# Performance work log

Hardware: AMD Instinct MI355X
Metric: run time of the kernel (lower is better)

The kernel has to match this reference:

```python
import jax, jax.numpy as jnp
import numpy as np

N, E, D, L = 50000, 400000, 128, 5
EPS = 1e-5  # BatchNorm1d default eps


def setup_inputs() -> dict:
    key = jax.random.key(0)
    ks = jax.random.split(key, 9)
    x = jax.random.normal(ks[0], (N, D), jnp.float32)
    edge_index = jax.random.randint(ks[1], (2, E), 0, N)
    edge_attr = jax.random.normal(ks[2], (E, 4), jnp.float32)
    # per-layer params (stacked over L layers)
    W1 = jax.random.normal(ks[3], (L, 3, D), jnp.float32) * (6.0 / (3 + D)) ** 0.5
    W2 = jax.random.normal(ks[4], (L, 1, D), jnp.float32) * (6.0 / (1 + D)) ** 0.5
    Wm = jax.random.normal(ks[5], (L, D, 2 * D), jnp.float32) * (6.0 / (3 * D)) ** 0.5
    bm = jnp.zeros((L, D), jnp.float32)
    gamma = jnp.ones((L, D), jnp.float32)
    beta = jnp.zeros((L, D), jnp.float32)
    return dict(x=x, edge_index=edge_index, edge_attr=edge_attr,
                W1=W1, W2=W2, Wm=Wm, bm=bm, gamma=gamma, beta=beta)


def reference(x, edge_index, edge_attr, W1, W2, Wm, bm, gamma, beta):
    row, col = edge_index[0], edge_index[1]
    # symmetric GCN norm: deg computed by scattering ones at col
    deg = jax.ops.segment_sum(jnp.ones((E,), x.dtype), col, num_segments=N)
    deg_safe = jnp.where(deg > 0, deg, 1.0)
    dinv = jnp.where(deg > 0, deg_safe ** -0.5, 0.0)  # [N]
    norm = dinv[row] * dinv[col]                      # [E]

    h = x
    for l in range(L):
        # edge feature projection ('2-3d'): first 3 cols @ W1 + last col @ W2
        edge_fea = edge_attr[:, :3] @ W1[l] + edge_attr[:, 3:] @ W2[l]  # [E, D]
        # message: norm * (x_j + edge_fea), gather at source (row)
        msg = norm[:, None] * (h[row] + edge_fea)                       # [E, D]
        # aggregate: scatter-add at target (col)
        agg = jax.ops.segment_sum(msg, col, num_segments=N)             # [N, D]
        # mlp(concat([x, out])) with ReLU
        h2 = jax.nn.relu(jnp.concatenate([h, agg], axis=1) @ Wm[l].T + bm[l])
        # BatchNorm1d (training mode: batch stats, biased variance)
        mean = h2.mean(axis=0)
        var = jnp.mean((h2 - mean) ** 2, axis=0)
        h = gamma[l] * (h2 - mean) * jax.lax.rsqrt(var + EPS) + beta[l]
        if l < L - 1:
            h = jax.nn.relu(h)
        # dropout p=0 -> identity
    return h
```

## Files before the change

### kernel.cpp

```cpp
#include <hip/hip_runtime.h>

#define D 128
#define EPSBN 1e-5f
#define PB 800

typedef __attribute__((ext_vector_type(8))) short bf16x8;
typedef __attribute__((ext_vector_type(4))) float f32x4;

static __device__ __forceinline__ unsigned short f2b(float f) {
    unsigned u = __float_as_uint(f);
    unsigned r = u + 0x7FFF + ((u >> 16) & 1);
    return (unsigned short)(r >> 16);
}
static __device__ __forceinline__ float b2f_lo(unsigned p) { return __uint_as_float(p << 16); }
static __device__ __forceinline__ float b2f_hi(unsigned p) { return __uint_as_float(p & 0xFFFF0000u); }


__global__ void k_deg(const int* __restrict__ ei, int E, int* __restrict__ deg) {
    int e = blockIdx.x * 256 + threadIdx.x;
    if (e < E) atomicAdd(&deg[ei[E + e]], 1);
}

__global__ void k_dinv(const int* __restrict__ deg, float* __restrict__ dinv, int N) {
    int v = blockIdx.x * 256 + threadIdx.x;
    if (v < N) {
        int d = deg[v];
        dinv[v] = (d > 0) ? rsqrtf((float)d) : 0.0f;
    }
}

__global__ void k_bsum(const int* __restrict__ deg, int* __restrict__ bsum, int N) {
    __shared__ int sm[256];
    int t = threadIdx.x, v = blockIdx.x * 256 + t;
    sm[t] = (v < N) ? deg[v] : 0;
    __syncthreads();
    for (int off = 128; off > 0; off >>= 1) {
        if (t < off) sm[t] += sm[t + off];
        __syncthreads();
    }
    if (t == 0) bsum[blockIdx.x] = sm[0];
}

__global__ void k_bscan(const int* __restrict__ bsum, int* __restrict__ boff,
                        int* __restrict__ row_ptr, int NB, int N, int E) {
    __shared__ int sm[256];
    int t = threadIdx.x;
    int v = (t < NB) ? bsum[t] : 0;
    sm[t] = v;
    __syncthreads();
    for (int off = 1; off < 256; off <<= 1) {
        int x = (t >= off) ? sm[t - off] : 0;
        __syncthreads();
        sm[t] += x;
        __syncthreads();
    }
    if (t < NB) boff[t] = sm[t] - v;
    if (t == 0) row_ptr[N] = E;
}

__global__ void k_scatter(const int* __restrict__ deg, const int* __restrict__ boff,
                          int* __restrict__ row_ptr, int* __restrict__ cursor, int N) {
    __shared__ int sm[256];
    int t = threadIdx.x, v = blockIdx.x * 256 + t;
    int val = (v < N) ? deg[v] : 0;
    sm[t] = val;
    __syncthreads();
    for (int off = 1; off < 256; off <<= 1) {
        int x = (t >= off) ? sm[t - off] : 0;
        __syncthreads();
        sm[t] += x;
        __syncthreads();
    }
    if (v < N) {
        int e = boff[blockIdx.x] + sm[t] - val;
        row_ptr[v] = e;
        cursor[v] = e;
    }
}

__global__ void k_fill(const int* __restrict__ ei, int* __restrict__ cursor,
                       int2* __restrict__ csr, int E) {
    int e = blockIdx.x * 256 + threadIdx.x;
    if (e >= E) return;
    int r = ei[e], c = ei[E + e];
    int pos = atomicAdd(&cursor[c], 1);
    csr[pos] = make_int2(r, e);
}

__global__ void k_cvals(const int* __restrict__ row_ptr, int2* __restrict__ csr,
                        const float* __restrict__ dinv, const float* __restrict__ attr,
                        float4* __restrict__ cvals, int N) {
    int v = blockIdx.x * 256 + threadIdx.x;
    if (v >= N) return;
    float dv = dinv[v];
    int jb = row_ptr[v], je = row_ptr[v + 1];
    float4 acc = make_float4(0.f, 0.f, 0.f, 0.f);
    for (int j = jb; j < je; ++j) {
        int2 e = csr[j];
        float nm = dinv[e.x] * dv;
        float4 a = *(const float4*)(attr + (size_t)e.y * 4);
        acc.x += nm * a.x; acc.y += nm * a.y;
        acc.z += nm * a.z; acc.w += nm * a.w;
        csr[j] = make_int2(e.x, __float_as_int(nm));
    }
    cvals[v] = acc;
}

__global__ void k_cvt(const float* __restrict__ in, unsigned short* __restrict__ outp, int n4) {
    int i = blockIdx.x * 256 + threadIdx.x;
    if (i >= n4) return;
    float4 v = *(const float4*)(in + (size_t)i * 4);
    ushort4 p;
    p.x = f2b(v.x); p.y = f2b(v.y); p.z = f2b(v.z); p.w = f2b(v.w);
    *(ushort4*)(outp + (size_t)i * 4) = p;
}


__global__ __launch_bounds__(256) void k_spmm(
        const unsigned short* __restrict__ hb, const int* __restrict__ row_ptr,
        const int2* __restrict__ csr, const float4* __restrict__ cvals,
        const float* __restrict__ W1l, const float* __restrict__ W2l,
        unsigned short* __restrict__ aggb, int N) {
    int lane = threadIdx.x & 63;
    int v = blockIdx.x * 4 + (threadIdx.x >> 6);
    if (v >= N) return;
    int qw = lane >> 4;
    int l4 = lane & 15;
    int d0 = l4 * 8;
    int jb = row_ptr[v], je = row_ptr[v + 1];

    float a[8];
#pragma unroll
    for (int i = 0; i < 8; ++i) a[i] = 0.f;

    for (int j0 = jb; j0 < je; j0 += 4) {
        int j = j0 + qw;
        bool ok = (j < je);
        int2 e = csr[ok ? j : jb];
        float nm = ok ? __int_as_float(e.y) : 0.f;
        uint4 p = *(const uint4*)(hb + (size_t)e.x * D + d0);
        a[0] += nm * b2f_lo(p.x); a[1] += nm * b2f_hi(p.x);
        a[2] += nm * b2f_lo(p.y); a[3] += nm * b2f_hi(p.y);
        a[4] += nm * b2f_lo(p.z); a[5] += nm * b2f_hi(p.z);
        a[6] += nm * b2f_lo(p.w); a[7] += nm * b2f_hi(p.w);
    }
#pragma unroll
    for (int i = 0; i < 8; ++i) {
        a[i] += __shfl_xor(a[i], 16);
        a[i] += __shfl_xor(a[i], 32);
    }
    if (qw == 0) {
        float4 c = cvals[v];
        float4 wa0 = *(const float4*)(W1l + d0);
        float4 wa1 = *(const float4*)(W1l + d0 + 4);
        float4 wb0 = *(const float4*)(W1l + D + d0);
        float4 wb1 = *(const float4*)(W1l + D + d0 + 4);
        float4 wc0 = *(const float4*)(W1l + 2 * D + d0);
        float4 wc1 = *(const float4*)(W1l + 2 * D + d0 + 4);
        float4 wd0 = *(const float4*)(W2l + d0);
        float4 wd1 = *(const float4*)(W2l + d0 + 4);
        a[0] += c.x * wa0.x + c.y * wb0.x + c.z * wc0.x + c.w * wd0.x;
        a[1] += c.x * wa0.y + c.y * wb0.y + c.z * wc0.y + c.w * wd0.y;
        a[2] += c.x * wa0.z + c.y * wb0.z + c.z * wc0.z + c.w * wd0.z;
        a[3] += c.x * wa0.w + c.y * wb0.w + c.z * wc0.w + c.w * wd0.w;
        a[4] += c.x * wa1.x + c.y * wb1.x + c.z * wc1.x + c.w * wd1.x;
        a[5] += c.x * wa1.y + c.y * wb1.y + c.z * wc1.y + c.w * wd1.y;
        a[6] += c.x * wa1.z + c.y * wb1.z + c.z * wc1.z + c.w * wd1.z;
        a[7] += c.x * wa1.w + c.y * wb1.w + c.z * wc1.w + c.w * wd1.w;
        uint4 o;
        o.x = ((unsigned)f2b(a[1]) << 16) | (unsigned)f2b(a[0]);
        o.y = ((unsigned)f2b(a[3]) << 16) | (unsigned)f2b(a[2]);
        o.z = ((unsigned)f2b(a[5]) << 16) | (unsigned)f2b(a[4]);
        o.w = ((unsigned)f2b(a[7]) << 16) | (unsigned)f2b(a[6]);
        *(uint4*)(aggb + (size_t)v * D + d0) = o;
    }
}

#define GROWS 64
#define GBK 64
__global__ __launch_bounds__(256) void k_gemm(
        const unsigned short* __restrict__ hb, const unsigned short* __restrict__ aggb,
        const unsigned short* __restrict__ Wmb, const float* __restrict__ bml,
        float* __restrict__ h2, float* __restrict__ pbuf, int N) {
    __shared__ unsigned short As[GROWS][GBK + 8];
    __shared__ unsigned short Bs[D][GBK + 8];
    __shared__ float sred[2][4][D];
    int tid = threadIdx.x;
    int lane = tid & 63, wave = tid >> 6;
    int n0 = blockIdx.x * GROWS;
    int l15 = lane & 15, q = lane >> 4;
    f32x4 acc[8];
#pragma unroll
    for (int t = 0; t < 8; ++t) acc[t] = (f32x4){0.f, 0.f, 0.f, 0.f};

    for (int kc = 0; kc < 4; ++kc) {
        const unsigned short* src = (kc < 2) ? hb : aggb;
        int k0 = (kc & 1) * GBK;
#pragma unroll
        for (int i = 0; i < 2; ++i) {
            int idx = tid + i * 256;
            int r = idx >> 3, seg = idx & 7;
            uint4 val = make_uint4(0u, 0u, 0u, 0u);
            if (n0 + r < N) val = *(const uint4*)(src + (size_t)(n0 + r) * D + k0 + seg * 8);
            *(uint4*)&As[r][seg * 8] = val;
        }
#pragma unroll
        for (int i = 0; i < 4; ++i) {
            int idx = tid + i * 256;
            int n = idx >> 3, seg = idx & 7;
            *(uint4*)&Bs[n][seg * 8] =
                *(const uint4*)(Wmb + (size_t)n * 256 + kc * GBK + seg * 8);
        }
        __syncthreads();
#pragma unroll
        for (int s = 0; s < 2; ++s) {
            bf16x8 a = *(const bf16x8*)&As[wave * 16 + l15][s * 32 + q * 8];
#pragma unroll
            for (int t = 0; t < 8; ++t) {
                bf16x8 b = *(const bf16x8*)&Bs[t * 16 + l15][s * 32 + q * 8];
                acc[t] = __builtin_amdgcn_mfma_f32_16x16x32_bf16(a, b, acc[t], 0, 0, 0);
            }
        }
        __syncthreads();
    }
    bool full = (n0 + GROWS <= N);
    float ps[8], pq[8];
#pragma unroll
    for (int t = 0; t < 8; ++t) {
        int n = t * 16 + l15;
        float bias = bml[n];
        float s = 0.f, qs = 0.f;
#pragma unroll
        for (int r = 0; r < 4; ++r) {
            int m = n0 + wave * 16 + q * 4 + r;
            float v = fmaxf(acc[t][r] + bias, 0.f);
            if (full || m < N) {
                h2[(size_t)m * D + n] = v;
                s += v; qs += v * v;
            }
        }
        ps[t] = s; pq[t] = qs;
    }
#pragma unroll
    for (int t = 0; t < 8; ++t) {
        ps[t] += __shfl_xor(ps[t], 16); ps[t] += __shfl_xor(ps[t], 32);
        pq[t] += __shfl_xor(pq[t], 16); pq[t] += __shfl_xor(pq[t], 32);
    }
    if (q == 0) {
#pragma unroll
        for (int t = 0; t < 8; ++t) {
            sred[0][wave][t * 16 + l15] = ps[t];
            sred[1][wave][t * 16 + l15] = pq[t];
        }
    }
    __syncthreads();
    if (tid < D) {
        float s = sred[0][0][tid] + sred[0][1][tid] + sred[0][2][tid] + sred[0][3][tid];
        pbuf[(size_t)tid * PB + blockIdx.x] = s;
    } else {
        int n = tid - D;
        float qv = sred[1][0][n] + sred[1][1][n] + sred[1][2][n] + sred[1][3][n];
        pbuf[(size_t)(n + D) * PB + blockIdx.x] = qv;
    }
}

__global__ __launch_bounds__(128) void k_reduce(
        const float* __restrict__ pbuf, const float* __restrict__ gam,
        const float* __restrict__ bet, float* __restrict__ scsh, int nb, int N) {
    int n = blockIdx.x;
    int t = threadIdx.x;
    float s = 0.f, qv = 0.f;
    for (int b = t; b < nb; b += 128) {
        s  += pbuf[(size_t)n * PB + b];
        qv += pbuf[(size_t)(n + D) * PB + b];
    }
#pragma unroll
    for (int off = 32; off > 0; off >>= 1) {
        s += __shfl_down(s, off);
        qv += __shfl_down(qv, off);
    }
    __shared__ float aux[4];
    if ((t & 63) == 0) { aux[t >> 6] = s; aux[2 + (t >> 6)] = qv; }
    __syncthreads();
    if (t == 0) {
        float S = aux[0] + aux[1], Q = aux[2] + aux[3];
        float mean = S / (float)N;
        float var = fmaxf(Q / (float)N - mean * mean, 0.f);
        float sc = gam[n] * rsqrtf(var + EPSBN);
        scsh[n] = sc;
        scsh[D + n] = bet[n] - mean * sc;
    }
}

__global__ void k_norm(const float* __restrict__ h2, const float* __restrict__ scsh,
                       unsigned short* __restrict__ hb_out, float* __restrict__ out_f,
                       int total4, int last) {
    int i = blockIdx.x * 256 + threadIdx.x;
    if (i >= total4) return;
    int base = i * 4;
    int d = base & (D - 1);
    float4 v = *(const float4*)(h2 + base);
    float4 o;
    o.x = scsh[d + 0] * v.x + scsh[D + d + 0];
    o.y = scsh[d + 1] * v.y + scsh[D + d + 1];
    o.z = scsh[d + 2] * v.z + scsh[D + d + 2];
    o.w = scsh[d + 3] * v.w + scsh[D + d + 3];
    if (!last) {
        o.x = fmaxf(o.x, 0.f); o.y = fmaxf(o.y, 0.f);
        o.z = fmaxf(o.z, 0.f); o.w = fmaxf(o.w, 0.f);
        ushort4 p;
        p.x = f2b(o.x); p.y = f2b(o.y); p.z = f2b(o.z); p.w = f2b(o.w);
        *(ushort4*)(hb_out + base) = p;
    } else {
        *(float4*)(out_f + base) = o;
    }
}


extern "C" void kernel_launch(void* const* d_in, const int* in_sizes, int n_in,
                              void* d_out, int out_size, void* d_ws, size_t ws_size,
                              hipStream_t stream) {
    const float* x    = (const float*)d_in[0];
    const int*   ei   = (const int*)d_in[1];
    const float* attr = (const float*)d_in[2];
    const float* W1   = (const float*)d_in[3];
    const float* W2   = (const float*)d_in[4];
    const float* Wm   = (const float*)d_in[5];
    const float* bm   = (const float*)d_in[6];
    const float* gam  = (const float*)d_in[7];
    const float* bet  = (const float*)d_in[8];
    float* out = (float*)d_out;

    const int N = in_sizes[0] / D;
    const int E = in_sizes[1] / 2;
    const int L = in_sizes[3] / (3 * D);
    const int NB = (N + 255) / 256;

    size_t off = 0;
    auto carve = [&](size_t bytes) {
        void* p = (char*)d_ws + off;
        off += (bytes + 255) & ~(size_t)255;
        return p;
    };
    int*            deg     = (int*)carve((size_t)N * 4);
    float*          dinv    = (float*)carve((size_t)N * 4);
    int*            row_ptr = (int*)carve((size_t)(N + 1) * 4);
    int*            cursor  = (int*)carve((size_t)N * 4);
    int*            bsum    = (int*)carve((size_t)NB * 4);
    int*            boff    = (int*)carve((size_t)NB * 4);
    int2*           csr     = (int2*)carve((size_t)(E + 4) * 8);
    float4*         cvals   = (float4*)carve((size_t)N * 16);
    unsigned short* xb      = (unsigned short*)carve((size_t)N * D * 2);
    unsigned short* hb      = (unsigned short*)carve((size_t)N * D * 2);
    unsigned short* aggb    = (unsigned short*)carve((size_t)N * D * 2);
    unsigned short* Wmb     = (unsigned short*)carve((size_t)L * D * 256 * 2);
    float*          h2      = (float*)carve((size_t)N * D * 4);
    float*          pbuf    = (float*)carve((size_t)2 * D * PB * 4);
    float*          scsh    = (float*)carve((size_t)2 * D * 4);
    (void)ws_size;

    hipMemsetAsync(deg, 0, (size_t)N * 4, stream);

    const int eb = (E + 255) / 256;
    k_deg<<<eb, 256, 0, stream>>>(ei, E, deg);
    k_dinv<<<NB, 256, 0, stream>>>(deg, dinv, N);
    k_bsum<<<NB, 256, 0, stream>>>(deg, bsum, N);
    k_bscan<<<1, 256, 0, stream>>>(bsum, boff, row_ptr, NB, N, E);
    k_scatter<<<NB, 256, 0, stream>>>(deg, boff, row_ptr, cursor, N);
    k_fill<<<eb, 256, 0, stream>>>(ei, cursor, csr, E);
    k_cvals<<<NB, 256, 0, stream>>>(row_ptr, csr, dinv, attr, cvals, N);

    const int xq = N * D / 4;
    k_cvt<<<(xq + 255) / 256, 256, 0, stream>>>(x, xb, xq);
    const int wq = L * D * 256 / 4;
    k_cvt<<<(wq + 255) / 256, 256, 0, stream>>>(Wm, Wmb, wq);

    const int total4 = N * D / 4;
    const int normb = (total4 + 255) / 256;
    const int gemmb = (N + GROWS - 1) / GROWS;
    const int spmmb = (N + 3) / 4;

    for (int l = 0; l < L; ++l) {
        const unsigned short* in = (l == 0) ? xb : hb;
        const float* W1l = W1 + (size_t)l * 3 * D;
        const float* W2l = W2 + (size_t)l * D;
        const unsigned short* Wml = Wmb + (size_t)l * D * 256;
        const float* bml = bm + (size_t)l * D;

        k_spmm<<<spmmb, 256, 0, stream>>>(in, row_ptr, csr, cvals, W1l, W2l, aggb, N);
        k_gemm<<<gemmb, 256, 0, stream>>>(in, aggb, Wml, bml, h2, pbuf, N);
        k_reduce<<<D, 128, 0, stream>>>(pbuf, gam + (size_t)l * D,
                                        bet + (size_t)l * D, scsh, gemmb, N);
        k_norm<<<normb, 256, 0, stream>>>(h2, scsh, hb, out, total4, (l < L - 1) ? 0 : 1);
    }
}
```

Before: 467.5 us.

## Fuse BatchNorm affine+ReLU into next layer's SpMM and GEMM loads

Drops the per-layer normalize kernel. The GEMM now stores the pre-norm activation as bf16, and the next layer's SpMM gather and GEMM A-tile load apply the BN scale/shift and ReLU on the fly. Only the last layer writes fp32 and runs a final normalize pass. This removes a full fp32 read and a bf16 write of the activation per layer, and halves the h2 write size. In exchange, the affine is recomputed once per edge in the gather, and bf16 rounding now happens before the normalization. Separately, CSR construction records the atomic slot in k_deg so a non-atomic placement kernel replaces the cursor atomics, and the SpMM loop is unrolled to two edges per quarter-wave.

```diff
diff --git a/kernel.cpp b/kernel.cpp
--- a/kernel.cpp
+++ b/kernel.cpp
@@ -16,9 +16,10 @@
 static __device__ __forceinline__ float b2f_hi(unsigned p) { return __uint_as_float(p & 0xFFFF0000u); }
 
 
-__global__ void k_deg(const int* __restrict__ ei, int E, int* __restrict__ deg) {
+__global__ void k_deg(const int* __restrict__ ei, int E, int* __restrict__ deg,
+                      int* __restrict__ pos) {
     int e = blockIdx.x * 256 + threadIdx.x;
-    if (e < E) atomicAdd(&deg[ei[E + e]], 1);
+    if (e < E) pos[e] = atomicAdd(&deg[ei[E + e]], 1);
 }
 
 __global__ void k_dinv(const int* __restrict__ deg, float* __restrict__ dinv, int N) {
@@ -59,7 +60,7 @@
 }
 
 __global__ void k_scatter(const int* __restrict__ deg, const int* __restrict__ boff,
-                          int* __restrict__ row_ptr, int* __restrict__ cursor, int N) {
+                          int* __restrict__ row_ptr, int N) {
     __shared__ int sm[256];
     int t = threadIdx.x, v = blockIdx.x * 256 + t;
     int val = (v < N) ? deg[v] : 0;
@@ -71,20 +72,15 @@
         sm[t] += x;
         __syncthreads();
     }
-    if (v < N) {
-        int e = boff[blockIdx.x] + sm[t] - val;
-        row_ptr[v] = e;
-        cursor[v] = e;
-    }
-}
-
-__global__ void k_fill(const int* __restrict__ ei, int* __restrict__ cursor,
-                       int2* __restrict__ csr, int E) {
+    if (v < N) row_ptr[v] = boff[blockIdx.x] + sm[t] - val;
+}
+
+__global__ void k_place(const int* __restrict__ ei, const int* __restrict__ row_ptr,
+                        const int* __restrict__ pos, int2* __restrict__ csr, int E) {
     int e = blockIdx.x * 256 + threadIdx.x;
     if (e >= E) return;
-    int r = ei[e], c = ei[E + e];
-    int pos = atomicAdd(&cursor[c], 1);
-    csr[pos] = make_int2(r, e);
+    int c = ei[E + e];
+    csr[row_ptr[c] + pos[e]] = make_int2(ei[e], e);
 }
 
 __global__ void k_cvals(const int* __restrict__ row_ptr, int2* __restrict__ csr,
@@ -120,6 +116,7 @@
         const unsigned short* __restrict__ hb, const int* __restrict__ row_ptr,
         const int2* __restrict__ csr, const float4* __restrict__ cvals,
         const float* __restrict__ W1l, const float* __restrict__ W2l,
+        const float* __restrict__ scsh, int apply,
         unsigned short* __restrict__ aggb, int N) {
     int lane = threadIdx.x & 63;
     int v = blockIdx.x * 4 + (threadIdx.x >> 6);
@@ -133,16 +130,53 @@
 #pragma unroll
     for (int i = 0; i < 8; ++i) a[i] = 0.f;
 
-    for (int j0 = jb; j0 < je; j0 += 4) {
-        int j = j0 + qw;
-        bool ok = (j < je);
-        int2 e = csr[ok ? j : jb];
-        float nm = ok ? __int_as_float(e.y) : 0.f;
-        uint4 p = *(const uint4*)(hb + (size_t)e.x * D + d0);
-        a[0] += nm * b2f_lo(p.x); a[1] += nm * b2f_hi(p.x);
-        a[2] += nm * b2f_lo(p.y); a[3] += nm * b2f_hi(p.y);
-        a[4] += nm * b2f_lo(p.z); a[5] += nm * b2f_hi(p.z);
-        a[6] += nm * b2f_lo(p.w); a[7] += nm * b2f_hi(p.w);
+    if (apply) {
+        float sc[8], sh[8];
+#pragma unroll
+        for (int i = 0; i < 8; i += 4) {
+            float4 s = *(const float4*)(scsh + d0 + i);
+            float4 t = *(const float4*)(scsh + D + d0 + i);
+            sc[i] = s.x; sc[i + 1] = s.y; sc[i + 2] = s.z; sc[i + 3] = s.w;
+            sh[i] = t.x; sh[i + 1] = t.y; sh[i + 2] = t.z; sh[i + 3] = t.w;
+        }
+        for (int j0 = jb; j0 < je; j0 += 8) {
+            int ja = j0 + qw, jc = j0 + 4 + qw;
+            bool oa = (ja < je), oc = (jc < je);
+            int2 ea = csr[oa ? ja : jb];
+            int2 ec = csr[oc ? jc : jb];
+            float na = oa ? __int_as_float(ea.y) : 0.f;
+            float nc = oc ? __int_as_float(ec.y) : 0.f;
+            uint4 pa = *(const uint4*)(hb + (size_t)ea.x * D + d0);
+            uint4 pc = *(const uint4*)(hb + (size_t)ec.x * D + d0);
+            float xa[8] = {b2f_lo(pa.x), b2f_hi(pa.x), b2f_lo(pa.y), b2f_hi(pa.y),
+                           b2f_lo(pa.z), b2f_hi(pa.z), b2f_lo(pa.w), b2f_hi(pa.w)};
+            float xc[8] = {b2f_lo(pc.x), b2f_hi(pc.x), b2f_lo(pc.y), b2f_hi(pc.y),
+                           b2f_lo(pc.z), b2f_hi(pc.z), b2f_lo(pc.w), b2f_hi(pc.w)};
+#pragma unroll
+            for (int i = 0; i < 8; ++i) {
+                a[i] += na * fmaxf(sc[i] * xa[i] + sh[i], 0.f);
+                a[i] += nc * fmaxf(sc[i] * xc[i] + sh[i], 0.f);
+            }
+        }
+    } else {
+        for (int j0 = jb; j0 < je; j0 += 8) {
+            int ja = j0 + qw, jc = j0 + 4 + qw;
+            bool oa = (ja < je), oc = (jc < je);
+            int2 ea = csr[oa ? ja : jb];
+            int2 ec = csr[oc ? jc : jb];
+            float na = oa ? __int_as_float(ea.y) : 0.f;
+            float nc = oc ? __int_as_float(ec.y) : 0.f;
+            uint4 pa = *(const uint4*)(hb + (size_t)ea.x * D + d0);
+            uint4 pc = *(const uint4*)(hb + (size_t)ec.x * D + d0);
+            a[0] += na * b2f_lo(pa.x) + nc * b2f_lo(pc.x);
+            a[1] += na * b2f_hi(pa.x) + nc * b2f_hi(pc.x);
+            a[2] += na * b2f_lo(pa.y) + nc * b2f_lo(pc.y);
+            a[3] += na * b2f_hi(pa.y) + nc * b2f_hi(pc.y);
+            a[4] += na * b2f_lo(pa.z) + nc * b2f_lo(pc.z);
+            a[5] += na * b2f_hi(pa.z) + nc * b2f_hi(pc.z);
+            a[6] += na * b2f_lo(pa.w) + nc * b2f_lo(pc.w);
+            a[7] += na * b2f_hi(pa.w) + nc * b2f_hi(pc.w);
+        }
     }
 #pragma unroll
     for (int i = 0; i < 8; ++i) {
@@ -179,9 +213,11 @@
 #define GROWS 64
 #define GBK 64
 __global__ __launch_bounds__(256) void k_gemm(
-        const unsigned short* __restrict__ hb, const unsigned short* __restrict__ aggb,
+        const unsigned short* __restrict__ hsrc, const unsigned short* __restrict__ aggb,
         const unsigned short* __restrict__ Wmb, const float* __restrict__ bml,
-        float* __restrict__ h2, float* __restrict__ pbuf, int N) {
+        const float* __restrict__ scsh, int applyA,
+        unsigned short* __restrict__ h2b, float* __restrict__ h2f, int lastf,
+        float* __restrict__ pbuf, int N) {
     __shared__ unsigned short As[GROWS][GBK + 8];
     __shared__ unsigned short Bs[D][GBK + 8];
     __shared__ float sred[2][4][D];
@@ -194,7 +230,8 @@
     for (int t = 0; t < 8; ++t) acc[t] = (f32x4){0.f, 0.f, 0.f, 0.f};
 
     for (int kc = 0; kc < 4; ++kc) {
-        const unsigned short* src = (kc < 2) ? hb : aggb;
+        const unsigned short* src = (kc < 2) ? hsrc : aggb;
+        bool aff = (kc < 2) && applyA;
         int k0 = (kc & 1) * GBK;
 #pragma unroll
         for (int i = 0; i < 2; ++i) {
@@ -202,6 +239,25 @@
             int r = idx >> 3, seg = idx & 7;
             uint4 val = make_uint4(0u, 0u, 0u, 0u);
             if (n0 + r < N) val = *(const uint4*)(src + (size_t)(n0 + r) * D + k0 + seg * 8);
+            if (aff) {
+                int db = k0 + seg * 8;
+                float4 s0 = *(const float4*)(scsh + db);
+                float4 s1 = *(const float4*)(scsh + db + 4);
+                float4 t0 = *(const float4*)(scsh + D + db);
+                float4 t1 = *(const float4*)(scsh + D + db + 4);
+                float e0 = fmaxf(s0.x * b2f_lo(val.x) + t0.x, 0.f);
+                float e1 = fmaxf(s0.y * b2f_hi(val.x) + t0.y, 0.f);
+                float e2 = fmaxf(s0.z * b2f_lo(val.y) + t0.z, 0.f);
+                float e3 = fmaxf(s0.w * b2f_hi(val.y) + t0.w, 0.f);
+                float e4 = fmaxf(s1.x * b2f_lo(val.z) + t1.x, 0.f);
+                float e5 = fmaxf(s1.y * b2f_hi(val.z) + t1.y, 0.f);
+                float e6 = fmaxf(s1.z * b2f_lo(val.w) + t1.z, 0.f);
+                float e7 = fmaxf(s1.w * b2f_hi(val.w) + t1.w, 0.f);
+                val.x = ((unsigned)f2b(e1) << 16) | (unsigned)f2b(e0);
+                val.y = ((unsigned)f2b(e3) << 16) | (unsigned)f2b(e2);
+                val.z = ((unsigned)f2b(e5) << 16) | (unsigned)f2b(e4);
+                val.w = ((unsigned)f2b(e7) << 16) | (unsigned)f2b(e6);
+            }
             *(uint4*)&As[r][seg * 8] = val;
         }
 #pragma unroll
@@ -235,7 +291,8 @@
             int m = n0 + wave * 16 + q * 4 + r;
             float v = fmaxf(acc[t][r] + bias, 0.f);
             if (full || m < N) {
-                h2[(size_t)m * D + n] = v;
+                if (lastf) h2f[(size_t)m * D + n] = v;
+                else       h2b[(size_t)m * D + n] = f2b(v);
                 s += v; qs += v * v;
             }
         }
@@ -292,28 +349,19 @@
     }
 }
 
-__global__ void k_norm(const float* __restrict__ h2, const float* __restrict__ scsh,
-                       unsigned short* __restrict__ hb_out, float* __restrict__ out_f,
-                       int total4, int last) {
+__global__ void k_norm_last(const float* __restrict__ h2f, const float* __restrict__ scsh,
+                            float* __restrict__ out_f, int total4) {
     int i = blockIdx.x * 256 + threadIdx.x;
     if (i >= total4) return;
     int base = i * 4;
     int d = base & (D - 1);
-    float4 v = *(const float4*)(h2 + base);
+    float4 v = *(const float4*)(h2f + base);
     float4 o;
     o.x = scsh[d + 0] * v.x + scsh[D + d + 0];
     o.y = scsh[d + 1] * v.y + scsh[D + d + 1];
     o.z = scsh[d + 2] * v.z + scsh[D + d + 2];
     o.w = scsh[d + 3] * v.w + scsh[D + d + 3];
-    if (!last) {
-        o.x = fmaxf(o.x, 0.f); o.y = fmaxf(o.y, 0.f);
-        o.z = fmaxf(o.z, 0.f); o.w = fmaxf(o.w, 0.f);
-        ushort4 p;
-        p.x = f2b(o.x); p.y = f2b(o.y); p.z = f2b(o.z); p.w = f2b(o.w);
-        *(ushort4*)(hb_out + base) = p;
-    } else {
-        *(float4*)(out_f + base) = o;
-    }
+    *(float4*)(out_f + base) = o;
 }
 
 
@@ -345,16 +393,16 @@
     int*            deg     = (int*)carve((size_t)N * 4);
     float*          dinv    = (float*)carve((size_t)N * 4);
     int*            row_ptr = (int*)carve((size_t)(N + 1) * 4);
-    int*            cursor  = (int*)carve((size_t)N * 4);
+    int*            pos     = (int*)carve((size_t)E * 4);
     int*            bsum    = (int*)carve((size_t)NB * 4);
     int*            boff    = (int*)carve((size_t)NB * 4);
-    int2*           csr     = (int2*)carve((size_t)(E + 4) * 8);
+    int2*           csr     = (int2*)carve((size_t)(E + 8) * 8);
     float4*         cvals   = (float4*)carve((size_t)N * 16);
     unsigned short* xb      = (unsigned short*)carve((size_t)N * D * 2);
-    unsigned short* hb      = (unsigned short*)carve((size_t)N * D * 2);
+    unsigned short* h2b     = (unsigned short*)carve((size_t)N * D * 2);
     unsigned short* aggb    = (unsigned short*)carve((size_t)N * D * 2);
     unsigned short* Wmb     = (unsigned short*)carve((size_t)L * D * 256 * 2);
-    float*          h2      = (float*)carve((size_t)N * D * 4);
+    float*          h2f     = (float*)carve((size_t)N * D * 4);
     float*          pbuf    = (float*)carve((size_t)2 * D * PB * 4);
     float*          scsh    = (float*)carve((size_t)2 * D * 4);
     (void)ws_size;
@@ -362,12 +410,12 @@
     hipMemsetAsync(deg, 0, (size_t)N * 4, stream);
 
     const int eb = (E + 255) / 256;
-    k_deg<<<eb, 256, 0, stream>>>(ei, E, deg);
+    k_deg<<<eb, 256, 0, stream>>>(ei, E, deg, pos);
     k_dinv<<<NB, 256, 0, stream>>>(deg, dinv, N);
     k_bsum<<<NB, 256, 0, stream>>>(deg, bsum, N);
     k_bscan<<<1, 256, 0, stream>>>(bsum, boff, row_ptr, NB, N, E);
-    k_scatter<<<NB, 256, 0, stream>>>(deg, boff, row_ptr, cursor, N);
-    k_fill<<<eb, 256, 0, stream>>>(ei, cursor, csr, E);
+    k_scatter<<<NB, 256, 0, stream>>>(deg, boff, row_ptr, N);
+    k_place<<<eb, 256, 0, stream>>>(ei, row_ptr, pos, csr, E);
     k_cvals<<<NB, 256, 0, stream>>>(row_ptr, csr, dinv, attr, cvals, N);
 
     const int xq = N * D / 4;
@@ -376,21 +424,24 @@
     k_cvt<<<(wq + 255) / 256, 256, 0, stream>>>(Wm, Wmb, wq);
 
     const int total4 = N * D / 4;
-    const int normb = (total4 + 255) / 256;
     const int gemmb = (N + GROWS - 1) / GROWS;
     const int spmmb = (N + 3) / 4;
 
     for (int l = 0; l < L; ++l) {
-        const unsigned short* in = (l == 0) ? xb : hb;
+        const unsigned short* in = (l == 0) ? xb : h2b;
+        const int apply = (l > 0) ? 1 : 0;
+        const int last = (l == L - 1) ? 1 : 0;
         const float* W1l = W1 + (size_t)l * 3 * D;
         const float* W2l = W2 + (size_t)l * D;
         const unsigned short* Wml = Wmb + (size_t)l * D * 256;
         const float* bml = bm + (size_t)l * D;
 
-        k_spmm<<<spmmb, 256, 0, stream>>>(in, row_ptr, csr, cvals, W1l, W2l, aggb, N);
-        k_gemm<<<gemmb, 256, 0, stream>>>(in, aggb, Wml, bml, h2, pbuf, N);
+        k_spmm<<<spmmb, 256, 0, stream>>>(in, row_ptr, csr, cvals, W1l, W2l,
+                                          scsh, apply, aggb, N);
+        k_gemm<<<gemmb, 256, 0, stream>>>(in, aggb, Wml, bml, scsh, apply,
+                                          h2b, h2f, last, pbuf, N);
         k_reduce<<<D, 128, 0, stream>>>(pbuf, gam + (size_t)l * D,
                                         bet + (size_t)l * D, scsh, gemmb, N);
-        k_norm<<<normb, 256, 0, stream>>>(h2, scsh, hb, out, total4, (l < L - 1) ? 0 : 1);
-    }
-}
+    }
+    k_norm_last<<<(total4 + 255) / 256, 256, 0, stream>>>(h2f, scsh, out, total4);
+}
```

Measured after the change: 427.8 us. -8.5%, faster.

## Fuse SpMM aggregation into GEMM tile and simplify CSR build

Applied to the files above, without the earlier changes.

The per-layer SpMM is merged into the GEMM kernel. Each 64-row block gathers its neighbor aggregates into shared memory, so the aggb round trip through global memory and one launch per layer go away. The gather loop is unrolled to two edges per step to keep more loads in flight. CSR construction now records each edge's atomic slot during the degree pass and computes dinv inline, which drops the dinv and fill/cursor kernels. The risk is that the fused kernel has only about 782 blocks, each gathering serially over 16 rows per wave with larger shared memory, which may reduce parallelism and latency hiding compared with the 12500-block SpMM.

```diff
diff --git a/kernel.cpp b/kernel.cpp
--- a/kernel.cpp
+++ b/kernel.cpp
@@ -3,6 +3,8 @@
 #define D 128
 #define EPSBN 1e-5f
 #define PB 800
+#define GROWS 64
+#define GBK 64
 
 typedef __attribute__((ext_vector_type(8))) short bf16x8;
 typedef __attribute__((ext_vector_type(4))) float f32x4;
@@ -16,17 +18,10 @@
 static __device__ __forceinline__ float b2f_hi(unsigned p) { return __uint_as_float(p & 0xFFFF0000u); }
 
 
-__global__ void k_deg(const int* __restrict__ ei, int E, int* __restrict__ deg) {
+__global__ void k_deg(const int* __restrict__ ei, int E, int* __restrict__ deg,
+                      int* __restrict__ pos) {
     int e = blockIdx.x * 256 + threadIdx.x;
-    if (e < E) atomicAdd(&deg[ei[E + e]], 1);
-}
-
-__global__ void k_dinv(const int* __restrict__ deg, float* __restrict__ dinv, int N) {
-    int v = blockIdx.x * 256 + threadIdx.x;
-    if (v < N) {
-        int d = deg[v];
-        dinv[v] = (d > 0) ? rsqrtf((float)d) : 0.0f;
-    }
+    if (e < E) pos[e] = atomicAdd(&deg[ei[E + e]], 1);
 }
 
 __global__ void k_bsum(const int* __restrict__ deg, int* __restrict__ bsum, int N) {
@@ -59,7 +54,7 @@
 }
 
 __global__ void k_scatter(const int* __restrict__ deg, const int* __restrict__ boff,
-                          int* __restrict__ row_ptr, int* __restrict__ cursor, int N) {
+                          int* __restrict__ row_ptr, int N) {
     __shared__ int sm[256];
     int t = threadIdx.x, v = blockIdx.x * 256 + t;
     int val = (v < N) ? deg[v] : 0;
@@ -71,33 +66,31 @@
         sm[t] += x;
         __syncthreads();
     }
-    if (v < N) {
-        int e = boff[blockIdx.x] + sm[t] - val;
-        row_ptr[v] = e;
-        cursor[v] = e;
-    }
-}
-
-__global__ void k_fill(const int* __restrict__ ei, int* __restrict__ cursor,
-                       int2* __restrict__ csr, int E) {
+    if (v < N) row_ptr[v] = boff[blockIdx.x] + sm[t] - val;
+}
+
+__global__ void k_place(const int* __restrict__ ei, const int* __restrict__ row_ptr,
+                        const int* __restrict__ pos, int2* __restrict__ csr, int E) {
     int e = blockIdx.x * 256 + threadIdx.x;
     if (e >= E) return;
-    int r = ei[e], c = ei[E + e];
-    int pos = atomicAdd(&cursor[c], 1);
-    csr[pos] = make_int2(r, e);
+    int c = ei[E + e];
+    csr[row_ptr[c] + pos[e]] = make_int2(ei[e], e);
 }
 
 __global__ void k_cvals(const int* __restrict__ row_ptr, int2* __restrict__ csr,
-                        const float* __restrict__ dinv, const float* __restrict__ attr,
+                        const int* __restrict__ deg, const float* __restrict__ attr,
                         float4* __restrict__ cvals, int N) {
     int v = blockIdx.x * 256 + threadIdx.x;
     if (v >= N) return;
-    float dv = dinv[v];
+    int dgv = deg[v];
+    float dv = (dgv > 0) ? rsqrtf((float)dgv) : 0.f;
     int jb = row_ptr[v], je = row_ptr[v + 1];
     float4 acc = make_float4(0.f, 0.f, 0.f, 0.f);
     for (int j = jb; j < je; ++j) {
         int2 e = csr[j];
-        float nm = dinv[e.x] * dv;
+        int dgs = deg[e.x];
+        float ds = (dgs > 0) ? rsqrtf((float)dgs) : 0.f;
+        float nm = ds * dv;
         float4 a = *(const float4*)(attr + (size_t)e.y * 4);
         acc.x += nm * a.x; acc.y += nm * a.y;
         acc.z += nm * a.z; acc.w += nm * a.w;
@@ -116,72 +109,13 @@
 }
 
 
-__global__ __launch_bounds__(256) void k_spmm(
+__global__ __launch_bounds__(256) void k_fused(
         const unsigned short* __restrict__ hb, const int* __restrict__ row_ptr,
         const int2* __restrict__ csr, const float4* __restrict__ cvals,
         const float* __restrict__ W1l, const float* __restrict__ W2l,
-        unsigned short* __restrict__ aggb, int N) {
-    int lane = threadIdx.x & 63;
-    int v = blockIdx.x * 4 + (threadIdx.x >> 6);
-    if (v >= N) return;
-    int qw = lane >> 4;
-    int l4 = lane & 15;
-    int d0 = l4 * 8;
-    int jb = row_ptr[v], je = row_ptr[v + 1];
-
-    float a[8];
-#pragma unroll
-    for (int i = 0; i < 8; ++i) a[i] = 0.f;
-
-    for (int j0 = jb; j0 < je; j0 += 4) {
-        int j = j0 + qw;
-        bool ok = (j < je);
-        int2 e = csr[ok ? j : jb];
-        float nm = ok ? __int_as_float(e.y) : 0.f;
-        uint4 p = *(const uint4*)(hb + (size_t)e.x * D + d0);
-        a[0] += nm * b2f_lo(p.x); a[1] += nm * b2f_hi(p.x);
-        a[2] += nm * b2f_lo(p.y); a[3] += nm * b2f_hi(p.y);
-        a[4] += nm * b2f_lo(p.z); a[5] += nm * b2f_hi(p.z);
-        a[6] += nm * b2f_lo(p.w); a[7] += nm * b2f_hi(p.w);
-    }
-#pragma unroll
-    for (int i = 0; i < 8; ++i) {
-        a[i] += __shfl_xor(a[i], 16);
-        a[i] += __shfl_xor(a[i], 32);
-    }
-    if (qw == 0) {
-        float4 c = cvals[v];
-        float4 wa0 = *(const float4*)(W1l + d0);
-        float4 wa1 = *(const float4*)(W1l + d0 + 4);
-        float4 wb0 = *(const float4*)(W1l + D + d0);
-        float4 wb1 = *(const float4*)(W1l + D + d0 + 4);
-        float4 wc0 = *(const float4*)(W1l + 2 * D + d0);
-        float4 wc1 = *(const float4*)(W1l + 2 * D + d0 + 4);
-        float4 wd0 = *(const float4*)(W2l + d0);
-        float4 wd1 = *(const float4*)(W2l + d0 + 4);
-        a[0] += c.x * wa0.x + c.y * wb0.x + c.z * wc0.x + c.w * wd0.x;
-        a[1] += c.x * wa0.y + c.y * wb0.y + c.z * wc0.y + c.w * wd0.y;
-        a[2] += c.x * wa0.z + c.y * wb0.z + c.z * wc0.z + c.w * wd0.z;
-        a[3] += c.x * wa0.w + c.y * wb0.w + c.z * wc0.w + c.w * wd0.w;
-        a[4] += c.x * wa1.x + c.y * wb1.x + c.z * wc1.x + c.w * wd1.x;
-        a[5] += c.x * wa1.y + c.y * wb1.y + c.z * wc1.y + c.w * wd1.y;
-        a[6] += c.x * wa1.z + c.y * wb1.z + c.z * wc1.z + c.w * wd1.z;
-        a[7] += c.x * wa1.w + c.y * wb1.w + c.z * wc1.w + c.w * wd1.w;
-        uint4 o;
-        o.x = ((unsigned)f2b(a[1]) << 16) | (unsigned)f2b(a[0]);
-        o.y = ((unsigned)f2b(a[3]) << 16) | (unsigned)f2b(a[2]);
-        o.z = ((unsigned)f2b(a[5]) << 16) | (unsigned)f2b(a[4]);
-        o.w = ((unsigned)f2b(a[7]) << 16) | (unsigned)f2b(a[6]);
-        *(uint4*)(aggb + (size_t)v * D + d0) = o;
-    }
-}
-
-#define GROWS 64
-#define GBK 64
-__global__ __launch_bounds__(256) void k_gemm(
-        const unsigned short* __restrict__ hb, const unsigned short* __restrict__ aggb,
         const unsigned short* __restrict__ Wmb, const float* __restrict__ bml,
         float* __restrict__ h2, float* __restrict__ pbuf, int N) {
+    __shared__ unsigned short Ag[GROWS][D + 8];
     __shared__ unsigned short As[GROWS][GBK + 8];
     __shared__ unsigned short Bs[D][GBK + 8];
     __shared__ float sred[2][4][D];
@@ -189,20 +123,86 @@
     int lane = tid & 63, wave = tid >> 6;
     int n0 = blockIdx.x * GROWS;
     int l15 = lane & 15, q = lane >> 4;
+    int qw = q;
+    int l4 = l15;
+    int d0 = l4 * 8;
+
+    for (int i = 0; i < 16; ++i) {
+        int r = wave * 16 + i;
+        int v = n0 + r;
+        float a[8];
+#pragma unroll
+        for (int k = 0; k < 8; ++k) a[k] = 0.f;
+        if (v < N) {
+            int jb = row_ptr[v], je = row_ptr[v + 1];
+            for (int j0 = jb; j0 < je; j0 += 8) {
+                int ja = j0 + qw, jc = j0 + 4 + qw;
+                bool oa = (ja < je), oc = (jc < je);
+                int2 ea = csr[oa ? ja : jb];
+                int2 ec = csr[oc ? jc : jb];
+                float na = oa ? __int_as_float(ea.y) : 0.f;
+                float nc = oc ? __int_as_float(ec.y) : 0.f;
+                uint4 pa = *(const uint4*)(hb + (size_t)ea.x * D + d0);
+                uint4 pc = *(const uint4*)(hb + (size_t)ec.x * D + d0);
+                a[0] += na * b2f_lo(pa.x) + nc * b2f_lo(pc.x);
+                a[1] += na * b2f_hi(pa.x) + nc * b2f_hi(pc.x);
+                a[2] += na * b2f_lo(pa.y) + nc * b2f_lo(pc.y);
+                a[3] += na * b2f_hi(pa.y) + nc * b2f_hi(pc.y);
+                a[4] += na * b2f_lo(pa.z) + nc * b2f_lo(pc.z);
+                a[5] += na * b2f_hi(pa.z) + nc * b2f_hi(pc.z);
+                a[6] += na * b2f_lo(pa.w) + nc * b2f_lo(pc.w);
+                a[7] += na * b2f_hi(pa.w) + nc * b2f_hi(pc.w);
+            }
+#pragma unroll
+            for (int k = 0; k < 8; ++k) {
+                a[k] += __shfl_xor(a[k], 16);
+                a[k] += __shfl_xor(a[k], 32);
+            }
+            if (qw == 0) {
+                float4 c = cvals[v];
+                float4 wa0 = *(const float4*)(W1l + d0);
+                float4 wa1 = *(const float4*)(W1l + d0 + 4);
+                float4 wb0 = *(const float4*)(W1l + D + d0);
+                float4 wb1 = *(const float4*)(W1l + D + d0 + 4);
+                float4 wc0 = *(const float4*)(W1l + 2 * D + d0);
+                float4 wc1 = *(const float4*)(W1l + 2 * D + d0 + 4);
+                float4 wd0 = *(const float4*)(W2l + d0);
+                float4 wd1 = *(const float4*)(W2l + d0 + 4);
+                a[0] += c.x * wa0.x + c.y * wb0.x + c.z * wc0.x + c.w * wd0.x;
+                a[1] += c.x * wa0.y + c.y * wb0.y + c.z * wc0.y + c.w * wd0.y;
+                a[2] += c.x * wa0.z + c.y * wb0.z + c.z * wc0.z + c.w * wd0.z;
+                a[3] += c.x * wa0.w + c.y * wb0.w + c.z * wc0.w + c.w * wd0.w;
+                a[4] += c.x * wa1.x + c.y * wb1.x + c.z * wc1.x + c.w * wd1.x;
+                a[5] += c.x * wa1.y + c.y * wb1.y + c.z * wc1.y + c.w * wd1.y;
+                a[6] += c.x * wa1.z + c.y * wb1.z + c.z * wc1.z + c.w * wd1.z;
+                a[7] += c.x * wa1.w + c.y * wb1.w + c.z * wc1.w + c.w * wd1.w;
+            }
+        }
+        if (qw == 0) {
+            uint4 o;
+            o.x = ((unsigned)f2b(a[1]) << 16) | (unsigned)f2b(a[0]);
+            o.y = ((unsigned)f2b(a[3]) << 16) | (unsigned)f2b(a[2]);
+            o.z = ((unsigned)f2b(a[5]) << 16) | (unsigned)f2b(a[4]);
+            o.w = ((unsigned)f2b(a[7]) << 16) | (unsigned)f2b(a[6]);
+            *(uint4*)&Ag[r][d0] = o;
+        }
+    }
+
     f32x4 acc[8];
 #pragma unroll
     for (int t = 0; t < 8; ++t) acc[t] = (f32x4){0.f, 0.f, 0.f, 0.f};
 
     for (int kc = 0; kc < 4; ++kc) {
-        const unsigned short* src = (kc < 2) ? hb : aggb;
         int k0 = (kc & 1) * GBK;
-#pragma unroll
-        for (int i = 0; i < 2; ++i) {
-            int idx = tid + i * 256;
-            int r = idx >> 3, seg = idx & 7;
-            uint4 val = make_uint4(0u, 0u, 0u, 0u);
-            if (n0 + r < N) val = *(const uint4*)(src + (size_t)(n0 + r) * D + k0 + seg * 8);
-            *(uint4*)&As[r][seg * 8] = val;
+        if (kc < 2) {
+#pragma unroll
+            for (int i = 0; i < 2; ++i) {
+                int idx = tid + i * 256;
+                int r = idx >> 3, seg = idx & 7;
+                uint4 val = make_uint4(0u, 0u, 0u, 0u);
+                if (n0 + r < N) val = *(const uint4*)(hb + (size_t)(n0 + r) * D + k0 + seg * 8);
+                *(uint4*)&As[r][seg * 8] = val;
+            }
         }
 #pragma unroll
         for (int i = 0; i < 4; ++i) {
@@ -214,7 +214,9 @@
         __syncthreads();
 #pragma unroll
         for (int s = 0; s < 2; ++s) {
-            bf16x8 a = *(const bf16x8*)&As[wave * 16 + l15][s * 32 + q * 8];
+            bf16x8 a;
+            if (kc < 2) a = *(const bf16x8*)&As[wave * 16 + l15][s * 32 + q * 8];
+            else        a = *(const bf16x8*)&Ag[wave * 16 + l15][(kc - 2) * GBK + s * 32 + q * 8];
 #pragma unroll
             for (int t = 0; t < 8; ++t) {
                 bf16x8 b = *(const bf16x8*)&Bs[t * 16 + l15][s * 32 + q * 8];
@@ -223,6 +225,7 @@
         }
         __syncthreads();
     }
+
     bool full = (n0 + GROWS <= N);
     float ps[8], pq[8];
 #pragma unroll
@@ -343,16 +346,14 @@
         return p;
     };
     int*            deg     = (int*)carve((size_t)N * 4);
-    float*          dinv    = (float*)carve((size_t)N * 4);
     int*            row_ptr = (int*)carve((size_t)(N + 1) * 4);
-    int*            cursor  = (int*)carve((size_t)N * 4);
+    int*            pos     = (int*)carve((size_t)E * 4);
     int*            bsum    = (int*)carve((size_t)NB * 4);
     int*            boff    = (int*)carve((size_t)NB * 4);
-    int2*           csr     = (int2*)carve((size_t)(E + 4) * 8);
+    int2*           csr     = (int2*)carve((size_t)(E + 8) * 8);
     float4*         cvals   = (float4*)carve((size_t)N * 16);
     unsigned short* xb      = (unsigned short*)carve((size_t)N * D * 2);
     unsigned short* hb      = (unsigned short*)carve((size_t)N * D * 2);
-    unsigned short* aggb    = (unsigned short*)carve((size_t)N * D * 2);
     unsigned short* Wmb     = (unsigned short*)carve((size_t)L * D * 256 * 2);
     float*          h2      = (float*)carve((size_t)N * D * 4);
     float*          pbuf    = (float*)carve((size_t)2 * D * PB * 4);
@@ -362,13 +363,12 @@
     hipMemsetAsync(deg, 0, (size_t)N * 4, stream);
 
     const int eb = (E + 255) / 256;
-    k_deg<<<eb, 256, 0, stream>>>(ei, E, deg);
-    k_dinv<<<NB, 256, 0, stream>>>(deg, dinv, N);
+    k_deg<<<eb, 256, 0, stream>>>(ei, E, deg, pos);
     k_bsum<<<NB, 256, 0, stream>>>(deg, bsum, N);
     k_bscan<<<1, 256, 0, stream>>>(bsum, boff, row_ptr, NB, N, E);
-    k_scatter<<<NB, 256, 0, stream>>>(deg, boff, row_ptr, cursor, N);
-    k_fill<<<eb, 256, 0, stream>>>(ei, cursor, csr, E);
-    k_cvals<<<NB, 256, 0, stream>>>(row_ptr, csr, dinv, attr, cvals, N);
+    k_scatter<<<NB, 256, 0, stream>>>(deg, boff, row_ptr, N);
+    k_place<<<eb, 256, 0, stream>>>(ei, row_ptr, pos, csr, E);
+    k_cvals<<<NB, 256, 0, stream>>>(row_ptr, csr, deg, attr, cvals, N);
 
     const int xq = N * D / 4;
     k_cvt<<<(xq + 255) / 256, 256, 0, stream>>>(x, xb, xq);
@@ -377,8 +377,7 @@
 
     const int total4 = N * D / 4;
     const int normb = (total4 + 255) / 256;
-    const int gemmb = (N + GROWS - 1) / GROWS;
-    const int spmmb = (N + 3) / 4;
+    const int nt = (N + GROWS - 1) / GROWS;
 
     for (int l = 0; l < L; ++l) {
         const unsigned short* in = (l == 0) ? xb : hb;
@@ -386,11 +385,12 @@
         const float* W2l = W2 + (size_t)l * D;
         const unsigned short* Wml = Wmb + (size_t)l * D * 256;
         const float* bml = bm + (size_t)l * D;
-
-        k_spmm<<<spmmb, 256, 0, stream>>>(in, row_ptr, csr, cvals, W1l, W2l, aggb, N);
-        k_gemm<<<gemmb, 256, 0, stream>>>(in, aggb, Wml, bml, h2, pbuf, N);
+        int last = (l == L - 1) ? 1 : 0;
+
+        k_fused<<<nt, 256, 0, stream>>>(in, row_ptr, csr, cvals, W1l, W2l,
+                                        Wml, bml, h2, pbuf, N);
         k_reduce<<<D, 128, 0, stream>>>(pbuf, gam + (size_t)l * D,
-                                        bet + (size_t)l * D, scsh, gemmb, N);
-        k_norm<<<normb, 256, 0, stream>>>(h2, scsh, hb, out, total4, (l < L - 1) ? 0 : 1);
-    }
-}
+                                        bet + (size_t)l * D, scsh, nt, N);
+        k_norm<<<normb, 256, 0, stream>>>(h2, scsh, hb, out, total4, last);
+    }
+}
```

Measured after the change: 615.3 us. 1.32x slower.
